# Kernel tuning notes

Hardware: AMD Instinct MI355X
Metric: run time of the kernel (lower is better)

The kernel has to match this reference:

```python
import jax, jax.numpy as jnp
import numpy as np

N_TOKEN = 1024
N_I = 512
VOCAB = 10
D = 1024
L = 12
H_MLP = 4096
EPS = 1e-5  # torch LayerNorm default
B = 8


def layer_norm(x, g, b):
    mu = jnp.mean(x, axis=-1, keepdims=True)
    var = jnp.mean(jnp.square(x - mu), axis=-1, keepdims=True)
    return (x - mu) * jax.lax.rsqrt(var + EPS) * g + b


def setup_inputs() -> dict:
    key = jax.random.key(0)
    ks = jax.random.split(key, 12)
    s = 0.02  # init scale for weights
    return {
        'xt': jax.random.randint(ks[0], (B, N_TOKEN - N_I), 0, VOCAB),
        'zi': jax.random.randint(ks[1], (B, N_I), 0, VOCAB),
        'pos_emb': jax.random.normal(ks[2], (N_TOKEN, D), jnp.float32) * s,
        't_emb': jax.random.normal(ks[3], (VOCAB, D), jnp.float32) * s,
        'Wq': jax.random.normal(ks[4], (L, D, D), jnp.float32) * s,
        'Wk': jax.random.normal(ks[5], (L, D, D), jnp.float32) * s,
        'Wv': jax.random.normal(ks[6], (L, D, D), jnp.float32) * s,
        'ln1_g': jnp.ones((L, D), jnp.float32),
        'ln1_b': jnp.zeros((L, D), jnp.float32),
        'ln2_g': jnp.ones((L, D), jnp.float32),
        'ln2_b': jnp.zeros((L, D), jnp.float32),
        'mlp_w1': jax.random.normal(ks[7], (L, D, H_MLP), jnp.float32) * s,
        'mlp_b1': jnp.zeros((L, H_MLP), jnp.float32),
        'mlp_w2': jax.random.normal(ks[8], (L, H_MLP, D), jnp.float32) * s,
        'mlp_b2': jnp.zeros((L, D), jnp.float32),
        'ro_w': jax.random.normal(ks[9], (D, 1), jnp.float32) * s,
        'ro_b': jnp.zeros((1,), jnp.float32),
    }


def _forward(xt, zi, pos_emb, t_emb, Wq, Wk, Wv, ln1_g, ln1_b, ln2_g, ln2_b,
             mlp_w1, mlp_b1, mlp_w2, mlp_b2, ro_w, ro_b):
    # token embeddings: image tokens get -(c - zi)^2/2 in the first VOCAB dims, 0 elsewhere
    opts = jnp.arange(VOCAB, dtype=jnp.float32)
    leave = -jnp.square(opts[None, None, :] - zi[:, :, None].astype(jnp.float32)) * 0.5  # [B, N_I, V]
    emb_i = jnp.pad(leave, ((0, 0), (0, 0), (0, D - VOCAB)))  # [B, N_I, D]
    emb_t = t_emb[xt]                                          # [B, T1, D]
    H = jnp.concatenate([emb_i, emb_t], axis=1) + pos_emb[None, :, :]  # [B, T, D]

    inv_sqrt_d = np.float32(1.0 / np.sqrt(D))

    def step(H, p):
        wq, wk, wv, g1, b1, g2, b2, w1, bb1, w2, bb2 = p
        H1 = layer_norm(H, g1, b1)
        q = H1 @ wq
        k = H1 @ wk
        v = H1 @ wv
        attn = jnp.einsum('bid,bjd->bij', q, k) * inv_sqrt_d  # [B, T, T]
        attn = jax.nn.softmax(attn, axis=-1)
        H = H + jnp.einsum('bij,bjd->bid', attn, v)
        H2 = layer_norm(H, g2, b2)
        # torch nn.GELU default is exact (erf) gelu
        H = H + (jax.nn.gelu(H2 @ w1 + bb1, approximate=False) @ w2 + bb2)
        return H, None

    H, _ = jax.lax.scan(step, H, (Wq, Wk, Wv, ln1_g, ln1_b, ln2_g, ln2_b,
                                  mlp_w1, mlp_b1, mlp_w2, mlp_b2))
    pred = H @ ro_w + ro_b  # [B, T, 1]
    return pred[:, :N_I, 0]  # [B, N_I]


def reference(xt, zi, pos_emb, t_emb, Wq, Wk, Wv, ln1_g, ln1_b, ln2_g, ln2_b,
              mlp_w1, mlp_b1, mlp_w2, mlp_b2, ro_w, ro_b):
    return _forward(xt, zi, pos_emb, t_emb, Wq, Wk, Wv, ln1_g, ln1_b, ln2_g, ln2_b,
                    mlp_w1, mlp_b1, mlp_w2, mlp_b2, ro_w, ro_b)
```

## Files before the change

kernel.cpp:

```cpp
#include <hip/hip_runtime.h>
#include <cstdint>
#include <cmath>

typedef unsigned short u16;
typedef unsigned int u32;
typedef short bf16x8 __attribute__((ext_vector_type(8)));
typedef float f32x4 __attribute__((ext_vector_type(4)));

#define DEV static __device__ __forceinline__

DEV u16 f2bf(float f) {
  union { float f; u32 u; } v; v.f = f;
  return (u16)((v.u + 0x7FFFu + ((v.u >> 16) & 1u)) >> 16);
}
DEV float bf2f(u32 lo16) {
  union { u32 u; float f; } v; v.u = lo16 << 16; return v.f;
}

DEV void gload16(const void* g, u16* l) {
  __builtin_amdgcn_global_load_lds(
      (const __attribute__((address_space(1))) void*)g,
      (__attribute__((address_space(3))) void*)l, 16, 0, 0);
}

template<int MODE>
__global__ __launch_bounds__(256)
void gemmA(const u16* __restrict__ A, const u16* __restrict__ Bt,
           void* __restrict__ Cv, const float* __restrict__ bias,
           int M, int N, int K, int ldA, int ldB,
           long sA, long sB, long sC, float scale)
{
  __shared__ __align__(16) u16 As[128 * 64];
  __shared__ __align__(16) u16 Bs[128 * 64];

  const int bz = blockIdx.z;
  const long m0 = (long)blockIdx.x * 128, n0 = (long)blockIdx.y * 128;
  const int t = threadIdx.x;
  const int wave = t >> 6, lane = t & 63;
  const int wr = (wave >> 1) * 64, wc = (wave & 1) * 64;
  const int lg = lane >> 4, lr = lane & 15;

  const long ldA2 = (long)ldA * 2, ldB2 = (long)ldB * 2;

  const int rl = lane >> 3, c7 = lane & 7;
  const int sb = (c7 * 16) ^ (rl << 4);
  const char* aP[4]; const char* bP[4];
  u16* aL[4]; u16* bL[4];
  {
    const char* Ab = (const char*)(A + (long)bz * sA);
    const char* Bb = (const char*)(Bt + (long)bz * sB);
    #pragma unroll
    for (int c = 0; c < 4; ++c) {
      const int q = c * 4 + wave;
      aP[c] = Ab + (m0 + q * 8 + rl) * ldA2 + sb;
      bP[c] = Bb + (n0 + q * 8 + rl) * ldB2 + sb;
      aL[c] = As + q * 512;
      bL[c] = Bs + q * 512;
    }
  }

  const int rswz = (lr & 7) << 4;
  auto rd = [&](const u16* base, int row, int cbyte) -> bf16x8 {
    return *reinterpret_cast<const bf16x8*>(
        reinterpret_cast<const char*>(base) + row * 128 + (cbyte ^ rswz));
  };

  f32x4 acc[4][4];
  #pragma unroll
  for (int i = 0; i < 4; ++i)
    #pragma unroll
    for (int j = 0; j < 4; ++j)
      acc[i][j] = (f32x4){0.f, 0.f, 0.f, 0.f};

  for (int k0 = 0; k0 < K; k0 += 64) {
    #pragma unroll
    for (int c = 0; c < 4; ++c) {
      gload16(aP[c], aL[c]);
      gload16(bP[c], bL[c]);
      aP[c] += 128; bP[c] += 128;
    }
    __syncthreads();

    #pragma unroll
    for (int ks = 0; ks < 2; ++ks) {
      bf16x8 a[4], b[4];
      #pragma unroll
      for (int i = 0; i < 4; ++i)
        a[i] = rd(As, wr + i * 16 + lr, ks * 64 + lg * 16);
      #pragma unroll
      for (int i = 0; i < 4; ++i)
        b[i] = rd(Bs, wc + i * 16 + lr, ks * 64 + lg * 16);
      #pragma unroll
      for (int mi = 0; mi < 4; ++mi)
        #pragma unroll
        for (int ni = 0; ni < 4; ++ni)
          acc[mi][ni] = __builtin_amdgcn_mfma_f32_16x16x32_bf16(a[mi], b[ni], acc[mi][ni], 0, 0, 0);
    }
    __syncthreads();
  }

  #pragma unroll
  for (int mi = 0; mi < 4; ++mi) {
    #pragma unroll
    for (int ni = 0; ni < 4; ++ni) {
      #pragma unroll
      for (int r = 0; r < 4; ++r) {
        const long grow = m0 + wr + mi * 16 + lg * 4 + r;
        const long gcol = n0 + wc + ni * 16 + lr;
        const float v = acc[mi][ni][r];
        if constexpr (MODE == 0) {
          u16* Cp = (u16*)Cv + (long)bz * sC;
          Cp[grow * N + gcol] = f2bf(v * scale);
        } else if constexpr (MODE == 2) {
          float* Cp = (float*)Cv + (long)bz * sC;
          Cp[grow * N + gcol] += v;
        } else if constexpr (MODE == 3) {
          u16* Cp = (u16*)Cv + (long)bz * sC;
          const float x = v + bias[gcol];
          const float ge = 0.5f * x * (1.0f + erff(x * 0.70710678118f));
          Cp[grow * N + gcol] = f2bf(ge);
        } else if constexpr (MODE == 4) {
          float* Cp = (float*)Cv + (long)bz * sC;
          const long idx = grow * N + gcol;
          Cp[idx] = Cp[idx] + v + bias[gcol];
        }
      }
    }
  }
}

template<int MODE>
__global__ __launch_bounds__(512, 4)
void gemm8(const u16* __restrict__ A, const u16* __restrict__ Bt,
           void* __restrict__ Cv, const float* __restrict__ bias,
           int M, int N, int K, int ldA, int ldB, float scale)
{
  __shared__ __align__(16) u16 As[128 * 64];
  __shared__ __align__(16) u16 Bs[128 * 64];

  const int nx = gridDim.x;
  const int nb = nx * gridDim.y;
  const int lid = blockIdx.x + nx * blockIdx.y;
  const int nid = (lid & 7) * (nb >> 3) + (lid >> 3);
  const long m0 = (long)(nid % nx) * 128;
  const long n0 = (long)(nid / nx) * 128;

  const int t = threadIdx.x;
  const int wave = t >> 6, lane = t & 63;
  const int wr = (wave >> 2) * 64, wc = (wave & 3) * 32;
  const int lg = lane >> 4, lr = lane & 15;

  const long ldA2 = (long)ldA * 2, ldB2 = (long)ldB * 2;

  const int rl = lane >> 3, c7 = lane & 7;
  const int sb = (c7 * 16) ^ (rl << 4);
  const char* aP[2]; const char* bP[2];
  u16* aL[2]; u16* bL[2];
  {
    const char* Ab = (const char*)A;
    const char* Bb = (const char*)Bt;
    #pragma unroll
    for (int c = 0; c < 2; ++c) {
      const int q = c * 8 + wave;
      aP[c] = Ab + (m0 + q * 8 + rl) * ldA2 + sb;
      bP[c] = Bb + (n0 + q * 8 + rl) * ldB2 + sb;
      aL[c] = As + q * 512;
      bL[c] = Bs + q * 512;
    }
  }

  const int rswz = (lr & 7) << 4;
  auto rd = [&](const u16* base, int row, int cbyte) -> bf16x8 {
    return *reinterpret_cast<const bf16x8*>(
        reinterpret_cast<const char*>(base) + row * 128 + (cbyte ^ rswz));
  };

  f32x4 acc[4][2];
  #pragma unroll
  for (int i = 0; i < 4; ++i)
    #pragma unroll
    for (int j = 0; j < 2; ++j)
      acc[i][j] = (f32x4){0.f, 0.f, 0.f, 0.f};

  for (int k0 = 0; k0 < K; k0 += 64) {
    #pragma unroll
    for (int c = 0; c < 2; ++c) {
      gload16(aP[c], aL[c]);
      gload16(bP[c], bL[c]);
      aP[c] += 128; bP[c] += 128;
    }
    __syncthreads();

    #pragma unroll
    for (int ks = 0; ks < 2; ++ks) {
      bf16x8 a[4], b[2];
      #pragma unroll
      for (int i = 0; i < 4; ++i)
        a[i] = rd(As, wr + i * 16 + lr, ks * 64 + lg * 16);
      #pragma unroll
      for (int i = 0; i < 2; ++i)
        b[i] = rd(Bs, wc + i * 16 + lr, ks * 64 + lg * 16);
      #pragma unroll
      for (int mi = 0; mi < 4; ++mi)
        #pragma unroll
        for (int ni = 0; ni < 2; ++ni)
          acc[mi][ni] = __builtin_amdgcn_mfma_f32_16x16x32_bf16(a[mi], b[ni], acc[mi][ni], 0, 0, 0);
    }
    __syncthreads();
  }

  #pragma unroll
  for (int mi = 0; mi < 4; ++mi) {
    #pragma unroll
    for (int ni = 0; ni < 2; ++ni) {
      #pragma unroll
      for (int r = 0; r < 4; ++r) {
        const long grow = m0 + wr + mi * 16 + lg * 4 + r;
        const long gcol = n0 + wc + ni * 16 + lr;
        const float v = acc[mi][ni][r];
        if constexpr (MODE == 0) {
          ((u16*)Cv)[grow * N + gcol] = f2bf(v * scale);
        } else if constexpr (MODE == 3) {
          const float x = v + bias[gcol];
          const float u2 = 1.59576912f * x * (1.f + 0.044715f * x * x);
          const float ge = x / (1.f + __expf(-u2));
          ((u16*)Cv)[grow * N + gcol] = f2bf(ge);
        } else if constexpr (MODE == 4) {
          float* Cp = (float*)Cv;
          const long idx = grow * N + gcol;
          Cp[idx] = Cp[idx] + v + bias[gcol];
        }
      }
    }
  }
}

__global__ __launch_bounds__(256)
void trans_k(const float* __restrict__ wq, const float* __restrict__ wk,
             const float* __restrict__ wv, const float* __restrict__ w1,
             const float* __restrict__ w2, u16* __restrict__ ob)
{
  __shared__ u16 T[64][68];
  const int b = blockIdx.x;
  const float* in; u16* out; int K, N, tk, tn;
  if (b < 768) {
    const int m = b >> 8, tt = b & 255;
    in = (m == 0) ? wq : (m == 1) ? wk : wv;
    out = ob + (long)m * 1048576L;
    K = 1024; N = 1024; tk = tt >> 4; tn = tt & 15;
  } else if (b < 1792) {
    const int tt = b - 768;
    in = w1; out = ob + 3L * 1048576L; K = 1024; N = 4096;
    tk = tt >> 6; tn = tt & 63;
  } else {
    const int tt = b - 1792;
    in = w2; out = ob + 7L * 1048576L; K = 4096; N = 1024;
    tk = tt >> 4; tn = tt & 15;
  }
  const int k0 = tk * 64, n0 = tn * 64;
  const int t = threadIdx.x;
  {
    const int r = t >> 2, cq = (t & 3) * 16;
    const float* src = in + (long)(k0 + r) * N + n0 + cq;
    #pragma unroll
    for (int q = 0; q < 4; ++q) {
      const float4 v = *reinterpret_cast<const float4*>(src + q * 4);
      T[r][cq + q * 4 + 0] = f2bf(v.x);
      T[r][cq + q * 4 + 1] = f2bf(v.y);
      T[r][cq + q * 4 + 2] = f2bf(v.z);
      T[r][cq + q * 4 + 3] = f2bf(v.w);
    }
  }
  __syncthreads();
  {
    const int n = t >> 2, kq2 = (t & 3) * 16;
    u16 tmp[16];
    #pragma unroll
    for (int j = 0; j < 16; ++j) tmp[j] = T[kq2 + j][n];
    uint4* dst = reinterpret_cast<uint4*>(out + (long)(n0 + n) * K + k0 + kq2);
    dst[0] = *reinterpret_cast<const uint4*>(&tmp[0]);
    dst[1] = *reinterpret_cast<const uint4*>(&tmp[8]);
  }
}

__global__ __launch_bounds__(256)
void embed_k(const int* __restrict__ xt, const int* __restrict__ zi,
             const float* __restrict__ pos, const float* __restrict__ temb,
             float* __restrict__ H)
{
  const int bt = blockIdx.x;
  const int b = bt >> 10, tk = bt & 1023;
  const int d = threadIdx.x * 4;
  const float4 p = reinterpret_cast<const float4*>(pos + (long)tk * 1024)[threadIdx.x];
  float4 v;
  if (tk < 512) {
    const float z = (float)zi[b * 512 + tk];
    const float c0 = (float)(d + 0) - z, c1 = (float)(d + 1) - z;
    const float c2 = (float)(d + 2) - z, c3 = (float)(d + 3) - z;
    v.x = (d + 0 < 10) ? -0.5f * c0 * c0 : 0.f;
    v.y = (d + 1 < 10) ? -0.5f * c1 * c1 : 0.f;
    v.z = (d + 2 < 10) ? -0.5f * c2 * c2 : 0.f;
    v.w = (d + 3 < 10) ? -0.5f * c3 * c3 : 0.f;
  } else {
    const float* te = temb + (long)xt[b * 512 + (tk - 512)] * 1024;
    v = reinterpret_cast<const float4*>(te)[threadIdx.x];
  }
  float4 o; o.x = v.x + p.x; o.y = v.y + p.y; o.z = v.z + p.z; o.w = v.w + p.w;
  reinterpret_cast<float4*>(H + (long)bt * 1024)[threadIdx.x] = o;
}

__global__ __launch_bounds__(256)
void ln_k(const float* __restrict__ X, const float* __restrict__ g,
          const float* __restrict__ bta, u16* __restrict__ Y)
{
  __shared__ float sm[8];
  const long row = blockIdx.x;
  const float4 x = reinterpret_cast<const float4*>(X + row * 1024)[threadIdx.x];
  float s1 = x.x + x.y + x.z + x.w;
  float s2 = x.x * x.x + x.y * x.y + x.z * x.z + x.w * x.w;
  #pragma unroll
  for (int o = 32; o > 0; o >>= 1) { s1 += __shfl_down(s1, o); s2 += __shfl_down(s2, o); }
  const int w = threadIdx.x >> 6, ln = threadIdx.x & 63;
  if (ln == 0) { sm[w] = s1; sm[4 + w] = s2; }
  __syncthreads();
  s1 = sm[0] + sm[1] + sm[2] + sm[3];
  s2 = sm[4] + sm[5] + sm[6] + sm[7];
  const float mu = s1 * (1.f / 1024.f);
  const float var = s2 * (1.f / 1024.f) - mu * mu;
  const float inv = rsqrtf(var + 1e-5f);
  const float4 gg = reinterpret_cast<const float4*>(g)[threadIdx.x];
  const float4 bb = reinterpret_cast<const float4*>(bta)[threadIdx.x];
  const u32 o0 = (u32)f2bf((x.x - mu) * inv * gg.x + bb.x) | ((u32)f2bf((x.y - mu) * inv * gg.y + bb.y) << 16);
  const u32 o1 = (u32)f2bf((x.z - mu) * inv * gg.z + bb.z) | ((u32)f2bf((x.w - mu) * inv * gg.w + bb.w) << 16);
  reinterpret_cast<uint2*>(Y + row * 1024)[threadIdx.x] = make_uint2(o0, o1);
}

__global__ __launch_bounds__(256)
void sm_k(const u16* __restrict__ S, u16* __restrict__ P)
{
  __shared__ float sm[8];
  const long row = blockIdx.x;
  const uint2 raw = reinterpret_cast<const uint2*>(S + row * 1024)[threadIdx.x];
  const float x0 = bf2f(raw.x & 0xffffu), x1 = bf2f(raw.x >> 16);
  const float x2 = bf2f(raw.y & 0xffffu), x3 = bf2f(raw.y >> 16);
  float m = fmaxf(fmaxf(x0, x1), fmaxf(x2, x3));
  #pragma unroll
  for (int o = 32; o > 0; o >>= 1) m = fmaxf(m, __shfl_down(m, o));
  const int w = threadIdx.x >> 6, ln = threadIdx.x & 63;
  if (ln == 0) sm[w] = m;
  __syncthreads();
  m = fmaxf(fmaxf(sm[0], sm[1]), fmaxf(sm[2], sm[3]));
  const float e0 = __expf(x0 - m), e1 = __expf(x1 - m);
  const float e2 = __expf(x2 - m), e3 = __expf(x3 - m);
  float s = e0 + e1 + e2 + e3;
  #pragma unroll
  for (int o = 32; o > 0; o >>= 1) s += __shfl_down(s, o);
  if (ln == 0) sm[4 + w] = s;
  __syncthreads();
  const float tot = sm[4] + sm[5] + sm[6] + sm[7];
  const float r = 1.0f / tot;
  const u32 o0 = (u32)f2bf(e0 * r) | ((u32)f2bf(e1 * r) << 16);
  const u32 o1 = (u32)f2bf(e2 * r) | ((u32)f2bf(e3 * r) << 16);
  reinterpret_cast<uint2*>(P + row * 1024)[threadIdx.x] = make_uint2(o0, o1);
}

__global__ __launch_bounds__(256)
void ro_k(const float* __restrict__ H, const float* __restrict__ w,
          const float* __restrict__ b, float* __restrict__ out)
{
  __shared__ float sm[4];
  const int row = blockIdx.x;
  const int bb = row >> 9, i = row & 511;
  const float* h = H + ((long)bb * 1024 + i) * 1024;
  const float4 x = reinterpret_cast<const float4*>(h)[threadIdx.x];
  const float4 ww = reinterpret_cast<const float4*>(w)[threadIdx.x];
  float s = x.x * ww.x + x.y * ww.y + x.z * ww.z + x.w * ww.w;
  #pragma unroll
  for (int o = 32; o > 0; o >>= 1) s += __shfl_down(s, o);
  const int wv = threadIdx.x >> 6, ln = threadIdx.x & 63;
  if (ln == 0) sm[wv] = s;
  __syncthreads();
  if (threadIdx.x == 0) out[row] = sm[0] + sm[1] + sm[2] + sm[3] + b[0];
}

extern "C" void kernel_launch(void* const* d_in, const int* in_sizes, int n_in,
                              void* d_out, int out_size, void* d_ws, size_t ws_size,
                              hipStream_t stream)
{
  const int* xt = (const int*)d_in[0];
  const int* zi = (const int*)d_in[1];
  const float* pos  = (const float*)d_in[2];
  const float* temb = (const float*)d_in[3];
  const float* Wq = (const float*)d_in[4];
  const float* Wk = (const float*)d_in[5];
  const float* Wv = (const float*)d_in[6];
  const float* ln1g = (const float*)d_in[7];
  const float* ln1b = (const float*)d_in[8];
  const float* ln2g = (const float*)d_in[9];
  const float* ln2b = (const float*)d_in[10];
  const float* w1 = (const float*)d_in[11];
  const float* b1 = (const float*)d_in[12];
  const float* w2 = (const float*)d_in[13];
  const float* b2 = (const float*)d_in[14];
  const float* row_w = (const float*)d_in[15];
  const float* row_b = (const float*)d_in[16];

  char* ws = (char*)d_ws;
  const long MB = 1024 * 1024;
  float* H   = (float*)(ws + 0);
  u16*   H1  = (u16*)(ws + 32 * MB);
  u16*   QK  = (u16*)(ws + 48 * MB);
  u16*   Vt  = (u16*)(ws + 80 * MB);
  u16*   S   = (u16*)(ws + 96 * MB);
  u16*   P   = (u16*)(ws + 112 * MB);
  u16*   G   = (u16*)(ws + 80 * MB);
  u16*   WT  = (u16*)(ws + 144 * MB);

  u16* WvT = WT + 2 * 1048576L;
  u16* W1T = WT + 3 * 1048576L;
  u16* W2T = WT + 7 * 1048576L;

  const long s1M = 1024L * 1024L;
  const long s2M = 2L * 1024L * 1024L;

  embed_k<<<8192, 256, 0, stream>>>(xt, zi, pos, temb, H);

  for (int l = 0; l < 12; ++l) {
    const float* wq = Wq + (long)l * s1M;
    const float* wk = Wk + (long)l * s1M;
    const float* wv = Wv + (long)l * s1M;
    const float* mw1 = w1 + (long)l * 1024L * 4096L;
    const float* mb1 = b1 + (long)l * 4096L;
    const float* mw2 = w2 + (long)l * 4096L * 1024L;
    const float* mb2 = b2 + (long)l * 1024L;

    trans_k<<<2816, 256, 0, stream>>>(wq, wk, wv, mw1, mw2, WT);

    ln_k<<<8192, 256, 0, stream>>>(H, ln1g + l * 1024, ln1b + l * 1024, H1);

    gemm8<0><<<dim3(64, 16, 1), 512, 0, stream>>>(H1, WT, QK, nullptr,
        8192, 2048, 1024, 1024, 1024, 1.f);
    gemmA<0><<<dim3(8, 8, 8), 256, 0, stream>>>(WvT, H1, Vt, nullptr,
        1024, 1024, 1024, 1024, 1024, 0, s1M, s1M, 1.f);

    gemmA<0><<<dim3(8, 8, 8), 256, 0, stream>>>(QK, QK + 1024, S, nullptr,
        1024, 1024, 1024, 2048, 2048, s2M, s2M, s1M, 1.f / 32.f);

    sm_k<<<8192, 256, 0, stream>>>(S, P);

    gemmA<2><<<dim3(8, 8, 8), 256, 0, stream>>>(P, Vt, (void*)H, nullptr,
        1024, 1024, 1024, 1024, 1024, s1M, s1M, s1M, 1.f);

    ln_k<<<8192, 256, 0, stream>>>(H, ln2g + l * 1024, ln2b + l * 1024, H1);

    gemm8<3><<<dim3(64, 32, 1), 512, 0, stream>>>(H1, W1T, G, mb1,
        8192, 4096, 1024, 1024, 1024, 1.f);
    gemm8<4><<<dim3(64, 8, 1), 512, 0, stream>>>(G, W2T, (void*)H, mb2,
        8192, 1024, 4096, 4096, 4096, 1.f);
  }

  ro_k<<<4096, 256, 0, stream>>>(H, row_w, row_b, (float*)d_out);
}
```

Before: 4.304 ms.

## Fuse V projection into QK GEMM and deepen K tiles to 128

```diff
diff --git a/kernel.cpp b/kernel.cpp
--- a/kernel.cpp
+++ b/kernel.cpp
@@ -24,26 +24,138 @@
 }
 
 template<int MODE>
-__global__ __launch_bounds__(256)
-void gemmA(const u16* __restrict__ A, const u16* __restrict__ Bt,
+__global__ __launch_bounds__(512, 4)
+void gemm8(const u16* __restrict__ A, const u16* __restrict__ Bt,
            void* __restrict__ Cv, const float* __restrict__ bias,
-           int M, int N, int K, int ldA, int ldB,
-           long sA, long sB, long sC, float scale)
-{
-  __shared__ __align__(16) u16 As[128 * 64];
-  __shared__ __align__(16) u16 Bs[128 * 64];
+           u16* __restrict__ Vt, int M, int N, int K, int ldA, int ldB,
+           float scale)
+{
+  __shared__ __align__(16) u16 As[128 * 128];
+  __shared__ __align__(16) u16 Bs[128 * 128];
+
+  const int nx = gridDim.x;
+  const int nb = nx * gridDim.y;
+  const int lid = blockIdx.x + nx * blockIdx.y;
+  const int nid = (lid & 7) * (nb >> 3) + (lid >> 3);
+  const long m0 = (long)(nid % nx) * 128;
+  const long n0 = (long)(nid / nx) * 128;
+
+  const int t = threadIdx.x;
+  const int wave = t >> 6, lane = t & 63;
+  const int wr = (wave >> 2) * 64, wc = (wave & 3) * 32;
+  const int lg = lane >> 4, lr = lane & 15;
+
+  const long ldA2 = (long)ldA * 2, ldB2 = (long)ldB * 2;
+
+  const int rl = lane >> 4;
+  const int cb = (lane & 15) * 16;
+  const char* aP[4]; const char* bP[4];
+  u16* aL[4]; u16* bL[4];
+  {
+    const char* Ab = (const char*)A;
+    const char* Bb = (const char*)Bt;
+    #pragma unroll
+    for (int c = 0; c < 4; ++c) {
+      const int q = c * 8 + wave;
+      const int srow = q * 4 + rl;
+      const int sb = cb ^ ((srow & 7) << 4);
+      aP[c] = Ab + (m0 + srow) * ldA2 + sb;
+      bP[c] = Bb + (n0 + srow) * ldB2 + sb;
+      aL[c] = As + q * 512;
+      bL[c] = Bs + q * 512;
+    }
+  }
+
+  auto rd = [&](const u16* base, int row, int cbyte) -> bf16x8 {
+    return *reinterpret_cast<const bf16x8*>(
+        reinterpret_cast<const char*>(base) + row * 256 + (cbyte ^ ((row & 7) << 4)));
+  };
+
+  f32x4 acc[4][2];
+  #pragma unroll
+  for (int i = 0; i < 4; ++i)
+    #pragma unroll
+    for (int j = 0; j < 2; ++j)
+      acc[i][j] = (f32x4){0.f, 0.f, 0.f, 0.f};
+
+  for (int k0 = 0; k0 < K; k0 += 128) {
+    #pragma unroll
+    for (int c = 0; c < 4; ++c) {
+      gload16(aP[c], aL[c]);
+      gload16(bP[c], bL[c]);
+      aP[c] += 256; bP[c] += 256;
+    }
+    __syncthreads();
+
+    #pragma unroll
+    for (int ks = 0; ks < 4; ++ks) {
+      bf16x8 a[4], b[2];
+      #pragma unroll
+      for (int i = 0; i < 4; ++i)
+        a[i] = rd(As, wr + i * 16 + lr, ks * 64 + lg * 16);
+      #pragma unroll
+      for (int i = 0; i < 2; ++i)
+        b[i] = rd(Bs, wc + i * 16 + lr, ks * 64 + lg * 16);
+      #pragma unroll
+      for (int mi = 0; mi < 4; ++mi)
+        #pragma unroll
+        for (int ni = 0; ni < 2; ++ni)
+          acc[mi][ni] = __builtin_amdgcn_mfma_f32_16x16x32_bf16(a[mi], b[ni], acc[mi][ni], 0, 0, 0);
+    }
+    __syncthreads();
+  }
+
+  #pragma unroll
+  for (int mi = 0; mi < 4; ++mi) {
+    #pragma unroll
+    for (int ni = 0; ni < 2; ++ni) {
+      #pragma unroll
+      for (int r = 0; r < 4; ++r) {
+        const long grow = m0 + wr + mi * 16 + lg * 4 + r;
+        const long gcol = n0 + wc + ni * 16 + lr;
+        const float v = acc[mi][ni][r];
+        if constexpr (MODE == 3) {
+          const float x = v + bias[gcol];
+          const float u2 = 1.59576912f * x * (1.f + 0.044715f * x * x);
+          const float ge = x / (1.f + __expf(-u2));
+          ((u16*)Cv)[grow * N + gcol] = f2bf(ge);
+        } else if constexpr (MODE == 4) {
+          float* Cp = (float*)Cv;
+          const long idx = grow * N + gcol;
+          Cp[idx] = Cp[idx] + v + bias[gcol];
+        } else if constexpr (MODE == 5) {
+          if (gcol < 2048) {
+            ((u16*)Cv)[grow * 2048 + gcol] = f2bf(v * scale);
+          } else {
+            const long b = grow >> 10, tk = grow & 1023, d = gcol - 2048;
+            Vt[(b << 20) + (d << 10) + tk] = f2bf(v);
+          }
+        }
+      }
+    }
+  }
+}
+
+template<int MODE>
+__global__ __launch_bounds__(512, 4)
+void gemm8b(const u16* __restrict__ A, const u16* __restrict__ Bt,
+            void* __restrict__ Cv, int N, int K, int ldA, int ldB,
+            long sA, long sB, long sC, float scale)
+{
+  __shared__ __align__(16) u16 As[128 * 128];
+  __shared__ __align__(16) u16 Bs[128 * 128];
 
   const int bz = blockIdx.z;
   const long m0 = (long)blockIdx.x * 128, n0 = (long)blockIdx.y * 128;
   const int t = threadIdx.x;
   const int wave = t >> 6, lane = t & 63;
-  const int wr = (wave >> 1) * 64, wc = (wave & 1) * 64;
+  const int wr = (wave >> 2) * 64, wc = (wave & 3) * 32;
   const int lg = lane >> 4, lr = lane & 15;
 
   const long ldA2 = (long)ldA * 2, ldB2 = (long)ldB * 2;
 
-  const int rl = lane >> 3, c7 = lane & 7;
-  const int sb = (c7 * 16) ^ (rl << 4);
+  const int rl = lane >> 4;
+  const int cb = (lane & 15) * 16;
   const char* aP[4]; const char* bP[4];
   u16* aL[4]; u16* bL[4];
   {
@@ -51,49 +163,50 @@
     const char* Bb = (const char*)(Bt + (long)bz * sB);
     #pragma unroll
     for (int c = 0; c < 4; ++c) {
-      const int q = c * 4 + wave;
-      aP[c] = Ab + (m0 + q * 8 + rl) * ldA2 + sb;
-      bP[c] = Bb + (n0 + q * 8 + rl) * ldB2 + sb;
+      const int q = c * 8 + wave;
+      const int srow = q * 4 + rl;
+      const int sb = cb ^ ((srow & 7) << 4);
+      aP[c] = Ab + (m0 + srow) * ldA2 + sb;
+      bP[c] = Bb + (n0 + srow) * ldB2 + sb;
       aL[c] = As + q * 512;
       bL[c] = Bs + q * 512;
     }
   }
 
-  const int rswz = (lr & 7) << 4;
   auto rd = [&](const u16* base, int row, int cbyte) -> bf16x8 {
     return *reinterpret_cast<const bf16x8*>(
-        reinterpret_cast<const char*>(base) + row * 128 + (cbyte ^ rswz));
+        reinterpret_cast<const char*>(base) + row * 256 + (cbyte ^ ((row & 7) << 4)));
   };
 
-  f32x4 acc[4][4];
+  f32x4 acc[4][2];
   #pragma unroll
   for (int i = 0; i < 4; ++i)
     #pragma unroll
-    for (int j = 0; j < 4; ++j)
+    for (int j = 0; j < 2; ++j)
       acc[i][j] = (f32x4){0.f, 0.f, 0.f, 0.f};
 
-  for (int k0 = 0; k0 < K; k0 += 64) {
+  for (int k0 = 0; k0 < K; k0 += 128) {
     #pragma unroll
     for (int c = 0; c < 4; ++c) {
       gload16(aP[c], aL[c]);
       gload16(bP[c], bL[c]);
-      aP[c] += 128; bP[c] += 128;
+      aP[c] += 256; bP[c] += 256;
     }
     __syncthreads();
 
     #pragma unroll
-    for (int ks = 0; ks < 2; ++ks) {
-      bf16x8 a[4], b[4];
+    for (int ks = 0; ks < 4; ++ks) {
+      bf16x8 a[4], b[2];
       #pragma unroll
       for (int i = 0; i < 4; ++i)
         a[i] = rd(As, wr + i * 16 + lr, ks * 64 + lg * 16);
       #pragma unroll
-      for (int i = 0; i < 4; ++i)
+      for (int i = 0; i < 2; ++i)
         b[i] = rd(Bs, wc + i * 16 + lr, ks * 64 + lg * 16);
       #pragma unroll
       for (int mi = 0; mi < 4; ++mi)
         #pragma unroll
-        for (int ni = 0; ni < 4; ++ni)
+        for (int ni = 0; ni < 2; ++ni)
           acc[mi][ni] = __builtin_amdgcn_mfma_f32_16x16x32_bf16(a[mi], b[ni], acc[mi][ni], 0, 0, 0);
     }
     __syncthreads();
@@ -102,7 +215,7 @@
   #pragma unroll
   for (int mi = 0; mi < 4; ++mi) {
     #pragma unroll
-    for (int ni = 0; ni < 4; ++ni) {
+    for (int ni = 0; ni < 2; ++ni) {
       #pragma unroll
       for (int r = 0; r < 4; ++r) {
         const long grow = m0 + wr + mi * 16 + lg * 4 + r;
@@ -114,121 +227,6 @@
         } else if constexpr (MODE == 2) {
           float* Cp = (float*)Cv + (long)bz * sC;
           Cp[grow * N + gcol] += v;
-        } else if constexpr (MODE == 3) {
-          u16* Cp = (u16*)Cv + (long)bz * sC;
-          const float x = v + bias[gcol];
-          const float ge = 0.5f * x * (1.0f + erff(x * 0.70710678118f));
-          Cp[grow * N + gcol] = f2bf(ge);
-        } else if constexpr (MODE == 4) {
-          float* Cp = (float*)Cv + (long)bz * sC;
-          const long idx = grow * N + gcol;
-          Cp[idx] = Cp[idx] + v + bias[gcol];
-        }
-      }
-    }
-  }
-}
-
-template<int MODE>
-__global__ __launch_bounds__(512, 4)
-void gemm8(const u16* __restrict__ A, const u16* __restrict__ Bt,
-           void* __restrict__ Cv, const float* __restrict__ bias,
-           int M, int N, int K, int ldA, int ldB, float scale)
-{
-  __shared__ __align__(16) u16 As[128 * 64];
-  __shared__ __align__(16) u16 Bs[128 * 64];
-
-  const int nx = gridDim.x;
-  const int nb = nx * gridDim.y;
-  const int lid = blockIdx.x + nx * blockIdx.y;
-  const int nid = (lid & 7) * (nb >> 3) + (lid >> 3);
-  const long m0 = (long)(nid % nx) * 128;
-  const long n0 = (long)(nid / nx) * 128;
-
-  const int t = threadIdx.x;
-  const int wave = t >> 6, lane = t & 63;
-  const int wr = (wave >> 2) * 64, wc = (wave & 3) * 32;
-  const int lg = lane >> 4, lr = lane & 15;
-
-  const long ldA2 = (long)ldA * 2, ldB2 = (long)ldB * 2;
-
-  const int rl = lane >> 3, c7 = lane & 7;
-  const int sb = (c7 * 16) ^ (rl << 4);
-  const char* aP[2]; const char* bP[2];
-  u16* aL[2]; u16* bL[2];
-  {
-    const char* Ab = (const char*)A;
-    const char* Bb = (const char*)Bt;
-    #pragma unroll
-    for (int c = 0; c < 2; ++c) {
-      const int q = c * 8 + wave;
-      aP[c] = Ab + (m0 + q * 8 + rl) * ldA2 + sb;
-      bP[c] = Bb + (n0 + q * 8 + rl) * ldB2 + sb;
-      aL[c] = As + q * 512;
-      bL[c] = Bs + q * 512;
-    }
-  }
-
-  const int rswz = (lr & 7) << 4;
-  auto rd = [&](const u16* base, int row, int cbyte) -> bf16x8 {
-    return *reinterpret_cast<const bf16x8*>(
-        reinterpret_cast<const char*>(base) + row * 128 + (cbyte ^ rswz));
-  };
-
-  f32x4 acc[4][2];
-  #pragma unroll
-  for (int i = 0; i < 4; ++i)
-    #pragma unroll
-    for (int j = 0; j < 2; ++j)
-      acc[i][j] = (f32x4){0.f, 0.f, 0.f, 0.f};
-
-  for (int k0 = 0; k0 < K; k0 += 64) {
-    #pragma unroll
-    for (int c = 0; c < 2; ++c) {
-      gload16(aP[c], aL[c]);
-      gload16(bP[c], bL[c]);
-      aP[c] += 128; bP[c] += 128;
-    }
-    __syncthreads();
-
-    #pragma unroll
-    for (int ks = 0; ks < 2; ++ks) {
-      bf16x8 a[4], b[2];
-      #pragma unroll
-      for (int i = 0; i < 4; ++i)
-        a[i] = rd(As, wr + i * 16 + lr, ks * 64 + lg * 16);
-      #pragma unroll
-      for (int i = 0; i < 2; ++i)
-        b[i] = rd(Bs, wc + i * 16 + lr, ks * 64 + lg * 16);
-      #pragma unroll
-      for (int mi = 0; mi < 4; ++mi)
-        #pragma unroll
-        for (int ni = 0; ni < 2; ++ni)
-          acc[mi][ni] = __builtin_amdgcn_mfma_f32_16x16x32_bf16(a[mi], b[ni], acc[mi][ni], 0, 0, 0);
-    }
-    __syncthreads();
-  }
-
-  #pragma unroll
-  for (int mi = 0; mi < 4; ++mi) {
-    #pragma unroll
-    for (int ni = 0; ni < 2; ++ni) {
-      #pragma unroll
-      for (int r = 0; r < 4; ++r) {
-        const long grow = m0 + wr + mi * 16 + lg * 4 + r;
-        const long gcol = n0 + wc + ni * 16 + lr;
-        const float v = acc[mi][ni][r];
-        if constexpr (MODE == 0) {
-          ((u16*)Cv)[grow * N + gcol] = f2bf(v * scale);
-        } else if constexpr (MODE == 3) {
-          const float x = v + bias[gcol];
-          const float u2 = 1.59576912f * x * (1.f + 0.044715f * x * x);
-          const float ge = x / (1.f + __expf(-u2));
-          ((u16*)Cv)[grow * N + gcol] = f2bf(ge);
-        } else if constexpr (MODE == 4) {
-          float* Cp = (float*)Cv;
-          const long idx = grow * N + gcol;
-          Cp[idx] = Cp[idx] + v + bias[gcol];
         }
       }
     }
@@ -416,7 +414,6 @@
   u16*   G   = (u16*)(ws + 80 * MB);
   u16*   WT  = (u16*)(ws + 144 * MB);
 
-  u16* WvT = WT + 2 * 1048576L;
   u16* W1T = WT + 3 * 1048576L;
   u16* W2T = WT + 7 * 1048576L;
 
@@ -438,24 +435,22 @@
 
     ln_k<<<8192, 256, 0, stream>>>(H, ln1g + l * 1024, ln1b + l * 1024, H1);
 
-    gemm8<0><<<dim3(64, 16, 1), 512, 0, stream>>>(H1, WT, QK, nullptr,
-        8192, 2048, 1024, 1024, 1024, 1.f);
-    gemmA<0><<<dim3(8, 8, 8), 256, 0, stream>>>(WvT, H1, Vt, nullptr,
-        1024, 1024, 1024, 1024, 1024, 0, s1M, s1M, 1.f);
-
-    gemmA<0><<<dim3(8, 8, 8), 256, 0, stream>>>(QK, QK + 1024, S, nullptr,
-        1024, 1024, 1024, 2048, 2048, s2M, s2M, s1M, 1.f / 32.f);
+    gemm8<5><<<dim3(64, 24, 1), 512, 0, stream>>>(H1, WT, QK, nullptr, Vt,
+        8192, 3072, 1024, 1024, 1024, 1.f);
+
+    gemm8b<0><<<dim3(8, 8, 8), 512, 0, stream>>>(QK, QK + 1024, S,
+        1024, 1024, 2048, 2048, s2M, s2M, s1M, 1.f / 32.f);
 
     sm_k<<<8192, 256, 0, stream>>>(S, P);
 
-    gemmA<2><<<dim3(8, 8, 8), 256, 0, stream>>>(P, Vt, (void*)H, nullptr,
-        1024, 1024, 1024, 1024, 1024, s1M, s1M, s1M, 1.f);
+    gemm8b<2><<<dim3(8, 8, 8), 512, 0, stream>>>(P, Vt, (void*)H,
+        1024, 1024, 1024, 1024, s1M, s1M, s1M, 1.f);
 
     ln_k<<<8192, 256, 0, stream>>>(H, ln2g + l * 1024, ln2b + l * 1024, H1);
 
-    gemm8<3><<<dim3(64, 32, 1), 512, 0, stream>>>(H1, W1T, G, mb1,
+    gemm8<3><<<dim3(64, 32, 1), 512, 0, stream>>>(H1, W1T, G, mb1, nullptr,
         8192, 4096, 1024, 1024, 1024, 1.f);
-    gemm8<4><<<dim3(64, 8, 1), 512, 0, stream>>>(G, W2T, (void*)H, mb2,
+    gemm8<4><<<dim3(64, 8, 1), 512, 0, stream>>>(G, W2T, (void*)H, mb2, nullptr,
         8192, 1024, 4096, 4096, 4096, 1.f);
   }
 
```

After: 4.673 ms. 8.6% more time.
